# Performance work log

Measured on AMD Instinct MI355X. Metric: run time of the kernel, lower is better.

The kernel has to match this reference:

```python
import jax, jax.numpy as jnp
import numpy as np

DEPTH = 4
HEADS = 8
WINDOW = 256
RPW = 2                      # relay_tokens_per_window
SEQ_PER_RELAY = WINDOW // RPW  # 128 tokens per relay group
RELAY_START = 2              # depth_start_relay_attn (1-indexed layer number)
LN_EPS = 1e-5


def setup_inputs() -> dict:
    key = jax.random.key(0)
    ks = jax.random.split(key, 8)
    b, t, d, dff = 2, 2048, 512, 2048
    s = 0.02
    return {
        "x": jax.random.normal(ks[0], (b, t, d), dtype=jnp.float32),
        "relay_emb": jax.random.normal(ks[1], (1, d), dtype=jnp.float32) * s,
        "ln1_g": jnp.ones((DEPTH, d), jnp.float32),
        "ln1_b": jnp.zeros((DEPTH, d), jnp.float32),
        "loc_qkv_w": jax.random.normal(ks[2], (DEPTH, d, 3 * d), dtype=jnp.float32) * s,
        "loc_out_w": jax.random.normal(ks[3], (DEPTH, d, d), dtype=jnp.float32) * s,
        "loc_out_b": jnp.zeros((DEPTH, d), jnp.float32),
        "glob_qkv_w": jax.random.normal(ks[4], (DEPTH, d, 3 * d), dtype=jnp.float32) * s,
        "glob_out_w": jax.random.normal(ks[5], (DEPTH, d, d), dtype=jnp.float32) * s,
        "glob_out_b": jnp.zeros((DEPTH, d), jnp.float32),
        "ln2_g": jnp.ones((DEPTH, d), jnp.float32),
        "ln2_b": jnp.zeros((DEPTH, d), jnp.float32),
        "ff_w1": jax.random.normal(ks[6], (DEPTH, d, dff), dtype=jnp.float32) * s,
        "ff_b1": jnp.zeros((DEPTH, dff), jnp.float32),
        "ff_w2": jax.random.normal(ks[7], (DEPTH, dff, d), dtype=jnp.float32) * s,
        "ff_b2": jnp.zeros((DEPTH, d), jnp.float32),
    }


def _layernorm(x, g, b):
    m = jnp.mean(x, axis=-1, keepdims=True)
    v = jnp.mean(jnp.square(x - m), axis=-1, keepdims=True)
    return (x - m) * jax.lax.rsqrt(v + LN_EPS) * g + b


def _self_attention(x, qkv_w, out_w, out_b):
    # full (non-causal) multi-head attention, as in FullAttention
    b, t, d = x.shape
    h, dh = HEADS, d // HEADS
    q, k, v = jnp.split(x @ qkv_w, 3, axis=-1)
    mh = lambda u: u.reshape(b, t, h, dh).transpose(0, 2, 1, 3)  # b h t dh
    q, k, v = mh(q), mh(k), mh(v)
    dots = jnp.einsum('bhid,bhjd->bhij', q, k) * (dh ** -0.5)
    attn = jax.nn.softmax(dots, axis=-1)
    o = jnp.einsum('bhij,bhjd->bhid', attn, v)
    o = o.transpose(0, 2, 1, 3).reshape(b, t, d)
    return o @ out_w + out_b


def reference(x, relay_emb, ln1_g, ln1_b, loc_qkv_w, loc_out_w, loc_out_b,
              glob_qkv_w, glob_out_w, glob_out_b, ln2_g, ln2_b,
              ff_w1, ff_b1, ff_w2, ff_b2):
    b, t, d = x.shape
    # insert one relay token every SEQ_PER_RELAY tokens
    x = x.reshape(b, -1, SEQ_PER_RELAY, d)
    G = x.shape[1]
    rel = jnp.broadcast_to(relay_emb[None, None], (b, G, 1, d))
    x = jnp.concatenate([rel, x], axis=2).reshape(b, -1, d)  # (b, G*(129), d)

    for l in range(DEPTH):
        # attention block: PreNorm -> AttentionLayer, residual from sequence wrapper
        y = _layernorm(x, ln1_g[l], ln1_b[l])
        if (l + 1) >= RELAY_START:
            y = y.reshape(b, G, SEQ_PER_RELAY + 1, d)
            r = y[:, :, 0]                                       # (b, G, d) relay tokens
            r = _self_attention(r, glob_qkv_w[l], glob_out_w[l], glob_out_b[l]) + r
            y = jnp.concatenate([r[:, :, None], y[:, :, 1:]], axis=2).reshape(b, -1, d)
        x = x + _self_attention(y, loc_qkv_w[l], loc_out_w[l], loc_out_b[l])
        # feedforward block: PreNorm -> FFN with LeakyReLU(0.01)
        z = _layernorm(x, ln2_g[l], ln2_b[l])
        z = jax.nn.leaky_relu(z @ ff_w1[l] + ff_b1[l], negative_slope=0.01) @ ff_w2[l] + ff_b2[l]
        x = x + z

    # strip relay tokens
    x = x.reshape(b, G, SEQ_PER_RELAY + 1, d)
    return x[:, :, 1:].reshape(b, -1, d)
```

## Files before the change

### kernel.cpp

```cpp
#include <hip/hip_runtime.h>

typedef __attribute__((ext_vector_type(8))) __bf16 bf16x8;
typedef __attribute__((ext_vector_type(8))) unsigned short u16x8;
typedef __attribute__((ext_vector_type(4))) float f32x4;
typedef unsigned short u16;

#define TSEQ 2064
#define NTOK 4128
#define MPAD 4224

__device__ __forceinline__ float bf2f(u16 u) {
  unsigned x = ((unsigned)u) << 16;
  return __builtin_bit_cast(float, x);
}
__device__ __forceinline__ u16 f2bf(float f) {
  unsigned u = __builtin_bit_cast(unsigned, f);
  u += 0x7fffu + ((u >> 16) & 1u);
  return (u16)(u >> 16);
}

__device__ __forceinline__ void gll16(const u16* g, u16* l) {
  __builtin_amdgcn_global_load_lds((const __attribute__((address_space(1))) void*)g,
                                   (__attribute__((address_space(3))) void*)l, 16, 0, 0);
}
__device__ __forceinline__ int swz(int row, int col) {
  return row * 64 + (col ^ ((row & 7) << 3));
}

__global__ __launch_bounds__(256) void transpose_w(const float* __restrict__ src,
                                                   u16* __restrict__ dst,
                                                   int K, int N)
{
  __shared__ float tile[32][33];
  const int l = blockIdx.z;
  src += (size_t)l * K * N;
  dst += (size_t)l * K * N;
  const int n0 = blockIdx.x * 32, k0 = blockIdx.y * 32;
  const int c = threadIdx.x & 31, r = threadIdx.x >> 5;
#pragma unroll
  for (int rr = r; rr < 32; rr += 8)
    tile[rr][c] = src[(size_t)(k0 + rr) * N + n0 + c];
  __syncthreads();
#pragma unroll
  for (int rr = r; rr < 32; rr += 8)
    dst[(size_t)(n0 + rr) * K + k0 + c] = f2bf(tile[c][rr]);
}

__global__ void build_x(const float* __restrict__ xin, const float* __restrict__ relay,
                        float* __restrict__ xw)
{
  const int total = 2 * TSEQ * 512;
  for (int idx = blockIdx.x * 256 + threadIdx.x; idx < total; idx += gridDim.x * 256) {
    int col = idx & 511;
    int tok = (idx >> 9) % TSEQ;
    int b   = idx / (TSEQ * 512);
    int g = tok / 129, s = tok % 129;
    float v = (s == 0) ? relay[col]
                       : xin[((size_t)b * 2048 + g * 128 + (s - 1)) * 512 + col];
    xw[idx] = v;
  }
}

__global__ void extract_out(const float* __restrict__ xw, float* __restrict__ out)
{
  const int total = 2 * 2048 * 512;
  for (int idx = blockIdx.x * 256 + threadIdx.x; idx < total; idx += gridDim.x * 256) {
    int col = idx & 511;
    int tok = (idx >> 9) & 2047;
    int b   = idx / (2048 * 512);
    int g = tok >> 7, s = tok & 127;
    out[idx] = xw[((size_t)b * TSEQ + g * 129 + s + 1) * 512 + col];
  }
}

__global__ __launch_bounds__(256) void ln_kernel(const float* __restrict__ x,
                                                 const float* __restrict__ g,
                                                 const float* __restrict__ bta,
                                                 u16* __restrict__ y, int M)
{
  const int wid = threadIdx.x >> 6, lane = threadIdx.x & 63;
  const int row = blockIdx.x * 4 + wid;
  if (row >= M) return;
  const float* xr = x + (size_t)row * 512;
  float v[8];
  float s = 0.f;
#pragma unroll
  for (int j = 0; j < 8; ++j) { v[j] = xr[j * 64 + lane]; s += v[j]; }
#pragma unroll
  for (int m = 1; m <= 32; m <<= 1) s += __shfl_xor(s, m);
  float mean = s * (1.f / 512.f);
  float vs = 0.f;
#pragma unroll
  for (int j = 0; j < 8; ++j) { float d = v[j] - mean; vs += d * d; }
#pragma unroll
  for (int m = 1; m <= 32; m <<= 1) vs += __shfl_xor(vs, m);
  float rstd = rsqrtf(vs * (1.f / 512.f) + 1e-5f);
  u16* yr = y + (size_t)row * 512;
#pragma unroll
  for (int j = 0; j < 8; ++j) {
    int c = j * 64 + lane;
    yr[c] = f2bf((v[j] - mean) * rstd * g[c] + bta[c]);
  }
}

template<bool HAS_BIAS, bool ACT, bool RESID, bool OUT_BF16>
__global__ __launch_bounds__(256) void gemm2(
    const u16* __restrict__ A, const u16* __restrict__ Bt,
    const float* __restrict__ bias, const float* __restrict__ resid,
    void* __restrict__ outp, int M, int N, int K)
{
  __shared__ __attribute__((aligned(16))) u16 As[2][128 * 64];
  __shared__ __attribute__((aligned(16))) u16 Bs[2][128 * 64];
  const int tid = threadIdx.x, lane = tid & 63, wid = tid >> 6;
  const int row0 = blockIdx.x * 128, col0 = blockIdx.y * 128;
  const int wm = (wid >> 1) * 64, wn = (wid & 1) * 64;
  const int srow = tid >> 3, sseg = tid & 7;
  f32x4 acc[4][4];
#pragma unroll
  for (int m = 0; m < 4; ++m)
#pragma unroll
    for (int n = 0; n < 4; ++n) acc[m][n] = (f32x4)0.f;
  const u16* Ab = A + (size_t)row0 * K;
  const u16* Bb = Bt + (size_t)col0 * K;
#pragma unroll
  for (int i = 0; i < 4; ++i) {
    int row = srow + i * 32, ss = sseg ^ (row & 7);
    gll16(Ab + (size_t)row * K + ss * 8, &As[0][row * 64 + sseg * 8]);
    gll16(Bb + (size_t)row * K + ss * 8, &Bs[0][row * 64 + sseg * 8]);
  }
  const int fr = lane & 15, g = lane >> 4;
  int cur = 0;
  for (int k0 = 0; k0 < K; k0 += 64) {
    __syncthreads();
    if (k0 + 64 < K) {
      u16* ad = &As[cur ^ 1][0];
      u16* bd = &Bs[cur ^ 1][0];
#pragma unroll
      for (int i = 0; i < 4; ++i) {
        int row = srow + i * 32, ss = sseg ^ (row & 7);
        gll16(Ab + (size_t)row * K + k0 + 64 + ss * 8, ad + row * 64 + sseg * 8);
        gll16(Bb + (size_t)row * K + k0 + 64 + ss * 8, bd + row * 64 + sseg * 8);
      }
    }
    const u16* as_ = &As[cur][0];
    const u16* bs_ = &Bs[cur][0];
    bf16x8 a[2][4], bb[2][4];
#pragma unroll
    for (int kk = 0; kk < 2; ++kk) {
#pragma unroll
      for (int m = 0; m < 4; ++m) a[kk][m] = *(const bf16x8*)&as_[swz(wm + m * 16 + fr, kk * 32 + g * 8)];
#pragma unroll
      for (int n = 0; n < 4; ++n) bb[kk][n] = *(const bf16x8*)&bs_[swz(wn + n * 16 + fr, kk * 32 + g * 8)];
    }
    __builtin_amdgcn_s_setprio(1);
#pragma unroll
    for (int kk = 0; kk < 2; ++kk)
#pragma unroll
      for (int m = 0; m < 4; ++m)
#pragma unroll
        for (int n = 0; n < 4; ++n)
          acc[m][n] = __builtin_amdgcn_mfma_f32_16x16x32_bf16(a[kk][m], bb[kk][n], acc[m][n], 0, 0, 0);
    __builtin_amdgcn_s_setprio(0);
    cur ^= 1;
  }

  const int fg = lane >> 4;
#pragma unroll
  for (int m = 0; m < 4; ++m) {
#pragma unroll
    for (int n = 0; n < 4; ++n) {
#pragma unroll
      for (int j = 0; j < 4; ++j) {
        int grow = row0 + wm + m * 16 + fg * 4 + j;
        int gcol = col0 + wn + n * 16 + fr;
        if (grow < M) {
          float v = acc[m][n][j];
          if (HAS_BIAS) v += bias[gcol];
          if (ACT) v = (v > 0.f) ? v : 0.01f * v;
          if (RESID) v += resid[(size_t)grow * N + gcol];
          if (OUT_BF16) ((u16*)outp)[(size_t)grow * N + gcol] = f2bf(v);
          else ((float*)outp)[(size_t)grow * N + gcol] = v;
        }
      }
    }
  }
}

__global__ __launch_bounds__(256) void vtrans(const u16* __restrict__ big,
                                              u16* __restrict__ vg)
{
  __shared__ u16 t[64][72];
  const int tt = blockIdx.x;
  const int bh = blockIdx.y;
  const int b = bh >> 3, h = bh & 7;
  const int tid = threadIdx.x;
  const int srow = tid >> 3, sseg = tid & 7;
  const int t0 = tt * 64;
#pragma unroll
  for (int i = 0; i < 2; ++i) {
    int row = srow + i * 32;
    u16x8 v = *(const u16x8*)&big[((size_t)(b * TSEQ) + t0 + row) * 1536 + 1024 + h * 64 + sseg * 8];
    *(u16x8*)&t[row][sseg * 8] = v;
  }
  __syncthreads();
#pragma unroll
  for (int i = 0; i < 2; ++i) {
    int d = srow + i * 32;
    u16x8 v;
#pragma unroll
    for (int j = 0; j < 8; ++j) v[j] = t[sseg * 8 + j][d];
    *(u16x8*)&vg[((size_t)bh * 64 + d) * 2112 + t0 + sseg * 8] = v;
  }
}

__global__ __launch_bounds__(256) void flash_attn2(const u16* __restrict__ big,
                                                   const u16* __restrict__ vg,
                                                   u16* __restrict__ ob)
{
  __shared__ __attribute__((aligned(16))) u16 Qs[64 * 64];
  __shared__ __attribute__((aligned(16))) u16 Ks[2][64 * 64];
  __shared__ __attribute__((aligned(16))) u16 Vs[2][64 * 64];
  __shared__ __attribute__((aligned(16))) u16 Ps[4][16 * 64];
  const int tid = threadIdx.x, lane = tid & 63, wid = tid >> 6;
  const int qt = blockIdx.x, b = blockIdx.y >> 3, h = blockIdx.y & 7;
  const int q0 = qt * 64;
  const int srow = tid >> 3, sseg = tid & 7;

  const u16* qb = big + ((size_t)(b * TSEQ) + q0) * 1536 + h * 64;
  const u16* kb = big + ((size_t)(b * TSEQ)) * 1536 + h * 64 + 512;
  const u16* vb = vg + (size_t)blockIdx.y * 64 * 2112;
#pragma unroll
  for (int i = 0; i < 2; ++i) {
    int row = srow + i * 32, ss = sseg ^ (row & 7);
    gll16(qb + (size_t)row * 1536 + ss * 8, &Qs[row * 64 + sseg * 8]);
    gll16(kb + (size_t)row * 1536 + ss * 8, &Ks[0][row * 64 + sseg * 8]);
    gll16(vb + (size_t)row * 2112 + ss * 8, &Vs[0][row * 64 + sseg * 8]);
  }
  __syncthreads();
  const int fr = lane & 15, g = lane >> 4;
  bf16x8 aq0 = *(const bf16x8*)&Qs[swz(wid * 16 + fr, g * 8)];
  bf16x8 aq1 = *(const bf16x8*)&Qs[swz(wid * 16 + fr, 32 + g * 8)];

  f32x4 oacc[4];
#pragma unroll
  for (int nf = 0; nf < 4; ++nf) oacc[nf] = (f32x4)0.f;
  float mrow[4] = {-1e30f, -1e30f, -1e30f, -1e30f};
  float lsum[4] = {0.f, 0.f, 0.f, 0.f};
  int cur = 0;

  for (int kt = 0; kt < 33; ++kt) {
    if (kt + 1 < 33) {
      const u16* kb2 = kb + (size_t)(kt + 1) * 64 * 1536;
      const u16* vb2 = vb + (kt + 1) * 64;
      u16* kd = &Ks[cur ^ 1][0];
      u16* vd = &Vs[cur ^ 1][0];
#pragma unroll
      for (int i = 0; i < 2; ++i) {
        int row = srow + i * 32, ss = sseg ^ (row & 7);
        gll16(kb2 + (size_t)row * 1536 + ss * 8, kd + row * 64 + sseg * 8);
        gll16(vb2 + (size_t)row * 2112 + ss * 8, vd + row * 64 + sseg * 8);
      }
    }
    const u16* ks = &Ks[cur][0];
    const u16* vs = &Vs[cur][0];
    f32x4 s[4];
    __builtin_amdgcn_s_setprio(1);
#pragma unroll
    for (int n = 0; n < 4; ++n) {
      int row = n * 16 + fr;
      bf16x8 bk0 = *(const bf16x8*)&ks[swz(row, g * 8)];
      bf16x8 bk1 = *(const bf16x8*)&ks[swz(row, 32 + g * 8)];
      f32x4 t = (f32x4)0.f;
      t = __builtin_amdgcn_mfma_f32_16x16x32_bf16(aq0, bk0, t, 0, 0, 0);
      t = __builtin_amdgcn_mfma_f32_16x16x32_bf16(aq1, bk1, t, 0, 0, 0);
      s[n] = t;
    }
    __builtin_amdgcn_s_setprio(0);
#pragma unroll
    for (int n = 0; n < 4; ++n) {
      bool valid = (kt * 64 + n * 16 + fr) < TSEQ;
#pragma unroll
      for (int j = 0; j < 4; ++j) s[n][j] = valid ? s[n][j] * 0.125f : -1e30f;
    }
    float sc[4];
#pragma unroll
    for (int j = 0; j < 4; ++j) {
      float m0 = fmaxf(fmaxf(s[0][j], s[1][j]), fmaxf(s[2][j], s[3][j]));
#pragma unroll
      for (int d = 1; d <= 8; d <<= 1) m0 = fmaxf(m0, __shfl_xor(m0, d));
      float nm = fmaxf(mrow[j], m0);
      sc[j] = __expf(mrow[j] - nm);
      mrow[j] = nm;
      lsum[j] *= sc[j];
    }
#pragma unroll
    for (int nf = 0; nf < 4; ++nf)
#pragma unroll
      for (int j = 0; j < 4; ++j) oacc[nf][j] *= sc[j];

    float ps[4] = {0.f, 0.f, 0.f, 0.f};
#pragma unroll
    for (int n = 0; n < 4; ++n) {
#pragma unroll
      for (int j = 0; j < 4; ++j) {
        float p = __expf(s[n][j] - mrow[j]);
        ps[j] += p;
        Ps[wid][swz(g * 4 + j, n * 16 + fr)] = f2bf(p);
      }
    }
#pragma unroll
    for (int j = 0; j < 4; ++j) {
      float t = ps[j];
#pragma unroll
      for (int d = 1; d <= 8; d <<= 1) t += __shfl_xor(t, d);
      lsum[j] += t;
    }
    __builtin_amdgcn_s_setprio(1);
#pragma unroll
    for (int kc = 0; kc < 2; ++kc) {
      bf16x8 ap = *(const bf16x8*)&Ps[wid][swz(fr, kc * 32 + g * 8)];
#pragma unroll
      for (int nf = 0; nf < 4; ++nf) {
        bf16x8 bv = *(const bf16x8*)&vs[swz(nf * 16 + fr, kc * 32 + g * 8)];
        oacc[nf] = __builtin_amdgcn_mfma_f32_16x16x32_bf16(ap, bv, oacc[nf], 0, 0, 0);
      }
    }
    __builtin_amdgcn_s_setprio(0);
    __syncthreads();
    cur ^= 1;
  }

  float inv[4];
#pragma unroll
  for (int j = 0; j < 4; ++j) inv[j] = 1.f / lsum[j];
#pragma unroll
  for (int nf = 0; nf < 4; ++nf) {
#pragma unroll
    for (int j = 0; j < 4; ++j) {
      int row = q0 + wid * 16 + g * 4 + j;
      if (row < TSEQ)
        ob[((size_t)(b * TSEQ + row)) * 512 + h * 64 + nf * 16 + fr] = f2bf(oacc[nf][j] * inv[j]);
    }
  }
}

__global__ __launch_bounds__(256) void global_attn(const u16* __restrict__ rqkv,
                                                   u16* __restrict__ ro)
{
  const int b = blockIdx.x >> 3, h = blockIdx.x & 7;
  __shared__ float q[16][64], k[16][64], v[16][64], s[16][16], p[16][16];
  const int tid = threadIdx.x;
  for (int idx = tid; idx < 1024; idx += 256) {
    int rr = idx >> 6, c = idx & 63;
    size_t base = (size_t)(b * 16 + rr) * 1536 + h * 64 + c;
    q[rr][c] = bf2f(rqkv[base]);
    k[rr][c] = bf2f(rqkv[base + 512]);
    v[rr][c] = bf2f(rqkv[base + 1024]);
  }
  __syncthreads();
  {
    int i = tid >> 4, j = tid & 15;
    float acc = 0.f;
#pragma unroll
    for (int d = 0; d < 64; ++d) acc += q[i][d] * k[j][d];
    s[i][j] = acc * 0.125f;
  }
  __syncthreads();
  if (tid < 16) {
    float mx = -1e30f;
#pragma unroll
    for (int j = 0; j < 16; ++j) mx = fmaxf(mx, s[tid][j]);
    float sum = 0.f;
#pragma unroll
    for (int j = 0; j < 16; ++j) { float e = __expf(s[tid][j] - mx); p[tid][j] = e; sum += e; }
    float iv = 1.f / sum;
#pragma unroll
    for (int j = 0; j < 16; ++j) p[tid][j] *= iv;
  }
  __syncthreads();
  for (int idx = tid; idx < 1024; idx += 256) {
    int rr = idx >> 6, c = idx & 63;
    float acc = 0.f;
#pragma unroll
    for (int j = 0; j < 16; ++j) acc += p[rr][j] * v[j][c];
    ro[(size_t)(b * 16 + rr) * 512 + h * 64 + c] = f2bf(acc);
  }
}

__global__ void gather_relay(const u16* __restrict__ y, u16* __restrict__ rbuf)
{
  int idx = blockIdx.x * 256 + threadIdx.x;
  int col = idx & 511, rr = idx >> 9;
  int b = rr >> 4, g = rr & 15;
  rbuf[idx] = y[((size_t)b * TSEQ + g * 129) * 512 + col];
}

__global__ void relay_scatter(const float* __restrict__ rout, const u16* __restrict__ rbuf,
                              u16* __restrict__ y)
{
  int idx = blockIdx.x * 256 + threadIdx.x;
  int col = idx & 511, rr = idx >> 9;
  int b = rr >> 4, g = rr & 15;
  y[((size_t)b * TSEQ + g * 129) * 512 + col] = f2bf(rout[idx] + bf2f(rbuf[idx]));
}

extern "C" void kernel_launch(void* const* d_in, const int* in_sizes, int n_in,
                              void* d_out, int out_size, void* d_ws, size_t ws_size,
                              hipStream_t stream)
{
  const float* x_in     = (const float*)d_in[0];
  const float* rel_emb  = (const float*)d_in[1];
  const float* ln1_g    = (const float*)d_in[2];
  const float* ln1_b    = (const float*)d_in[3];
  const float* loc_qkv  = (const float*)d_in[4];
  const float* loc_ow   = (const float*)d_in[5];
  const float* loc_ob   = (const float*)d_in[6];
  const float* glob_qkv = (const float*)d_in[7];
  const float* glob_ow  = (const float*)d_in[8];
  const float* glob_ob  = (const float*)d_in[9];
  const float* ln2_g    = (const float*)d_in[10];
  const float* ln2_b    = (const float*)d_in[11];
  const float* ff_w1    = (const float*)d_in[12];
  const float* ff_b1    = (const float*)d_in[13];
  const float* ff_w2    = (const float*)d_in[14];
  const float* ff_b2    = (const float*)d_in[15];

  char* ws = (char*)d_ws;
  float* xbuf = (float*)(ws + 0);
  u16*   ybuf = (u16*)(ws + 8650752);
  u16*   obuf = (u16*)(ws + 12976128);
  u16*   big  = (u16*)(ws + 17301504);
  u16*   vg   = (u16*)(ws + 34603008);
  u16*   wLQ  = (u16*)(ws + 38928384);
  u16*   wGQ  = (u16*)(ws + 45219840);
  u16*   wLO  = (u16*)(ws + 51511296);
  u16*   wGO  = (u16*)(ws + 53608448);
  u16*   wF1  = (u16*)(ws + 55705600);
  u16*   wF2  = (u16*)(ws + 64094208);
  u16*   rbuf = (u16*)(ws + 72482816);
  u16*   rqkv = (u16*)(ws + 72613888);
  u16*   rov  = (u16*)(ws + 72712192);
  float* rout = (float*)(ws + 72843264);

  dim3 B(256);
  transpose_w<<<dim3(48, 16, 4), B, 0, stream>>>(loc_qkv, wLQ, 512, 1536);
  transpose_w<<<dim3(48, 16, 4), B, 0, stream>>>(glob_qkv, wGQ, 512, 1536);
  transpose_w<<<dim3(16, 16, 4), B, 0, stream>>>(loc_ow, wLO, 512, 512);
  transpose_w<<<dim3(16, 16, 4), B, 0, stream>>>(glob_ow, wGO, 512, 512);
  transpose_w<<<dim3(64, 16, 4), B, 0, stream>>>(ff_w1, wF1, 512, 2048);
  transpose_w<<<dim3(16, 64, 4), B, 0, stream>>>(ff_w2, wF2, 2048, 512);

  build_x<<<8256, B, 0, stream>>>(x_in, rel_emb, xbuf);

  for (int l = 0; l < 4; ++l) {
    ln_kernel<<<1032, B, 0, stream>>>(xbuf, ln1_g + l * 512, ln1_b + l * 512, ybuf, NTOK);
    if (l + 1 >= 2) {
      gather_relay<<<64, B, 0, stream>>>(ybuf, rbuf);
      gemm2<false, false, false, true><<<dim3(1, 12), B, 0, stream>>>(
          rbuf, wGQ + (size_t)l * 1536 * 512, nullptr, nullptr, rqkv, 32, 1536, 512);
      global_attn<<<16, B, 0, stream>>>(rqkv, rov);
      gemm2<true, false, false, false><<<dim3(1, 4), B, 0, stream>>>(
          rov, wGO + (size_t)l * 512 * 512, glob_ob + l * 512, nullptr, rout, 32, 512, 512);
      relay_scatter<<<64, B, 0, stream>>>(rout, rbuf, ybuf);
    }
    gemm2<false, false, false, true><<<dim3(33, 12), B, 0, stream>>>(
        ybuf, wLQ + (size_t)l * 1536 * 512, nullptr, nullptr, big, NTOK, 1536, 512);
    vtrans<<<dim3(33, 16), B, 0, stream>>>(big, vg);
    flash_attn2<<<dim3(33, 16), B, 0, stream>>>(big, vg, obuf);
    gemm2<true, false, true, false><<<dim3(33, 4), B, 0, stream>>>(
        obuf, wLO + (size_t)l * 512 * 512, loc_ob + l * 512, xbuf, xbuf, NTOK, 512, 512);
    ln_kernel<<<1032, B, 0, stream>>>(xbuf, ln2_g + l * 512, ln2_b + l * 512, ybuf, NTOK);
    gemm2<true, true, false, true><<<dim3(33, 16), B, 0, stream>>>(
        ybuf, wF1 + (size_t)l * 2048 * 512, ff_b1 + l * 2048, nullptr, big, NTOK, 2048, 512);
    gemm2<true, false, true, false><<<dim3(33, 4), B, 0, stream>>>(
        big, wF2 + (size_t)l * 512 * 2048, ff_b2 + l * 512, xbuf, xbuf, NTOK, 512, 2048);
  }
  extract_out<<<8192, B, 0, stream>>>(xbuf, (float*)d_out);
}
```

Baseline: 1.160 ms.

## Split flash attention over key range, fuse V transpose into QKV GEMM epilogue

The QKV projection GEMM now writes the V slice directly in transposed per-head layout, which removes the separate vtrans kernel. Flash attention is split into two halves along the key dimension (grid z=2), doubling the number of blocks. Each half writes unnormalized partial outputs plus per-row max and sum, and a new fa_combine kernel merges them. The softmax is reworked to compute S transposed (K as the A operand), so the row max and sum need fewer shuffles, and P is staged in the reused Q shared memory. The trade-offs are an extra combine pass, scattered 2-byte stores in the GEMM epilogue, and bf16 rounding of the unnormalized partial outputs.

```diff
diff --git a/kernel.cpp b/kernel.cpp
--- a/kernel.cpp
+++ b/kernel.cpp
@@ -2,6 +2,7 @@
 
 typedef __attribute__((ext_vector_type(8))) __bf16 bf16x8;
 typedef __attribute__((ext_vector_type(8))) unsigned short u16x8;
+typedef __attribute__((ext_vector_type(4))) unsigned short u16x4;
 typedef __attribute__((ext_vector_type(4))) float f32x4;
 typedef unsigned short u16;
 
@@ -103,11 +104,11 @@
   }
 }
 
-template<bool HAS_BIAS, bool ACT, bool RESID, bool OUT_BF16>
+template<bool HAS_BIAS, bool ACT, bool RESID, bool OUT_BF16, bool VOUT>
 __global__ __launch_bounds__(256) void gemm2(
     const u16* __restrict__ A, const u16* __restrict__ Bt,
     const float* __restrict__ bias, const float* __restrict__ resid,
-    void* __restrict__ outp, int M, int N, int K)
+    void* __restrict__ outp, u16* __restrict__ vgout, int M, int N, int K)
 {
   __shared__ __attribute__((aligned(16))) u16 As[2][128 * 64];
   __shared__ __attribute__((aligned(16))) u16 Bs[2][128 * 64];
@@ -164,92 +165,75 @@
     cur ^= 1;
   }
 
-  const int fg = lane >> 4;
 #pragma unroll
   for (int m = 0; m < 4; ++m) {
 #pragma unroll
     for (int n = 0; n < 4; ++n) {
 #pragma unroll
       for (int j = 0; j < 4; ++j) {
-        int grow = row0 + wm + m * 16 + fg * 4 + j;
+        int grow = row0 + wm + m * 16 + g * 4 + j;
         int gcol = col0 + wn + n * 16 + fr;
         if (grow < M) {
           float v = acc[m][n][j];
           if (HAS_BIAS) v += bias[gcol];
           if (ACT) v = (v > 0.f) ? v : 0.01f * v;
           if (RESID) v += resid[(size_t)grow * N + gcol];
-          if (OUT_BF16) ((u16*)outp)[(size_t)grow * N + gcol] = f2bf(v);
-          else ((float*)outp)[(size_t)grow * N + gcol] = v;
+          if (VOUT && gcol >= 1024) {
+            int hh = (gcol - 1024) >> 6, dd = gcol & 63;
+            int bb2 = grow >= TSEQ;
+            int tok = grow - bb2 * TSEQ;
+            vgout[((size_t)((bb2 * 8 + hh) * 64 + dd)) * 2112 + tok] = f2bf(v);
+          } else if (OUT_BF16) {
+            ((u16*)outp)[(size_t)grow * N + gcol] = f2bf(v);
+          } else {
+            ((float*)outp)[(size_t)grow * N + gcol] = v;
+          }
         }
       }
     }
   }
 }
 
-__global__ __launch_bounds__(256) void vtrans(const u16* __restrict__ big,
-                                              u16* __restrict__ vg)
-{
-  __shared__ u16 t[64][72];
-  const int tt = blockIdx.x;
-  const int bh = blockIdx.y;
-  const int b = bh >> 3, h = bh & 7;
-  const int tid = threadIdx.x;
-  const int srow = tid >> 3, sseg = tid & 7;
-  const int t0 = tt * 64;
-#pragma unroll
-  for (int i = 0; i < 2; ++i) {
-    int row = srow + i * 32;
-    u16x8 v = *(const u16x8*)&big[((size_t)(b * TSEQ) + t0 + row) * 1536 + 1024 + h * 64 + sseg * 8];
-    *(u16x8*)&t[row][sseg * 8] = v;
-  }
-  __syncthreads();
-#pragma unroll
-  for (int i = 0; i < 2; ++i) {
-    int d = srow + i * 32;
-    u16x8 v;
-#pragma unroll
-    for (int j = 0; j < 8; ++j) v[j] = t[sseg * 8 + j][d];
-    *(u16x8*)&vg[((size_t)bh * 64 + d) * 2112 + t0 + sseg * 8] = v;
-  }
-}
-
-__global__ __launch_bounds__(256) void flash_attn2(const u16* __restrict__ big,
+__global__ __launch_bounds__(256) void flash_attn3(const u16* __restrict__ big,
                                                    const u16* __restrict__ vg,
-                                                   u16* __restrict__ ob)
+                                                   u16* __restrict__ op0,
+                                                   u16* __restrict__ op1,
+                                                   float2* __restrict__ mlb)
 {
   __shared__ __attribute__((aligned(16))) u16 Qs[64 * 64];
   __shared__ __attribute__((aligned(16))) u16 Ks[2][64 * 64];
   __shared__ __attribute__((aligned(16))) u16 Vs[2][64 * 64];
-  __shared__ __attribute__((aligned(16))) u16 Ps[4][16 * 64];
   const int tid = threadIdx.x, lane = tid & 63, wid = tid >> 6;
-  const int qt = blockIdx.x, b = blockIdx.y >> 3, h = blockIdx.y & 7;
+  const int qt = blockIdx.x, bh = blockIdx.y, z = blockIdx.z;
+  const int b = bh >> 3, h = bh & 7;
   const int q0 = qt * 64;
   const int srow = tid >> 3, sseg = tid & 7;
+  const int ktbeg = z * 17, ktend = z ? 33 : 17;
 
   const u16* qb = big + ((size_t)(b * TSEQ) + q0) * 1536 + h * 64;
   const u16* kb = big + ((size_t)(b * TSEQ)) * 1536 + h * 64 + 512;
-  const u16* vb = vg + (size_t)blockIdx.y * 64 * 2112;
+  const u16* vb = vg + (size_t)bh * 64 * 2112;
 #pragma unroll
   for (int i = 0; i < 2; ++i) {
     int row = srow + i * 32, ss = sseg ^ (row & 7);
     gll16(qb + (size_t)row * 1536 + ss * 8, &Qs[row * 64 + sseg * 8]);
-    gll16(kb + (size_t)row * 1536 + ss * 8, &Ks[0][row * 64 + sseg * 8]);
-    gll16(vb + (size_t)row * 2112 + ss * 8, &Vs[0][row * 64 + sseg * 8]);
+    gll16(kb + (size_t)(ktbeg * 64 + row) * 1536 + ss * 8, &Ks[0][row * 64 + sseg * 8]);
+    gll16(vb + (size_t)row * 2112 + ktbeg * 64 + ss * 8, &Vs[0][row * 64 + sseg * 8]);
   }
   __syncthreads();
   const int fr = lane & 15, g = lane >> 4;
   bf16x8 aq0 = *(const bf16x8*)&Qs[swz(wid * 16 + fr, g * 8)];
   bf16x8 aq1 = *(const bf16x8*)&Qs[swz(wid * 16 + fr, 32 + g * 8)];
+  u16* Pw = &Qs[wid * 1024];
 
   f32x4 oacc[4];
 #pragma unroll
   for (int nf = 0; nf < 4; ++nf) oacc[nf] = (f32x4)0.f;
-  float mrow[4] = {-1e30f, -1e30f, -1e30f, -1e30f};
-  float lsum[4] = {0.f, 0.f, 0.f, 0.f};
+  float mrow = -1e30f, lsum = 0.f;
   int cur = 0;
 
-  for (int kt = 0; kt < 33; ++kt) {
-    if (kt + 1 < 33) {
+  for (int kt = ktbeg; kt < ktend; ++kt) {
+    if (kt + 1 < ktend) {
       const u16* kb2 = kb + (size_t)(kt + 1) * 64 * 1536;
       const u16* vb2 = vb + (kt + 1) * 64;
       u16* kd = &Ks[cur ^ 1][0];
@@ -268,57 +252,58 @@
 #pragma unroll
     for (int n = 0; n < 4; ++n) {
       int row = n * 16 + fr;
-      bf16x8 bk0 = *(const bf16x8*)&ks[swz(row, g * 8)];
-      bf16x8 bk1 = *(const bf16x8*)&ks[swz(row, 32 + g * 8)];
+      bf16x8 ak0 = *(const bf16x8*)&ks[swz(row, g * 8)];
+      bf16x8 ak1 = *(const bf16x8*)&ks[swz(row, 32 + g * 8)];
       f32x4 t = (f32x4)0.f;
-      t = __builtin_amdgcn_mfma_f32_16x16x32_bf16(aq0, bk0, t, 0, 0, 0);
-      t = __builtin_amdgcn_mfma_f32_16x16x32_bf16(aq1, bk1, t, 0, 0, 0);
+      t = __builtin_amdgcn_mfma_f32_16x16x32_bf16(ak0, aq0, t, 0, 0, 0);
+      t = __builtin_amdgcn_mfma_f32_16x16x32_bf16(ak1, aq1, t, 0, 0, 0);
       s[n] = t;
     }
     __builtin_amdgcn_s_setprio(0);
 #pragma unroll
     for (int n = 0; n < 4; ++n) {
-      bool valid = (kt * 64 + n * 16 + fr) < TSEQ;
-#pragma unroll
-      for (int j = 0; j < 4; ++j) s[n][j] = valid ? s[n][j] * 0.125f : -1e30f;
-    }
-    float sc[4];
-#pragma unroll
-    for (int j = 0; j < 4; ++j) {
-      float m0 = fmaxf(fmaxf(s[0][j], s[1][j]), fmaxf(s[2][j], s[3][j]));
-#pragma unroll
-      for (int d = 1; d <= 8; d <<= 1) m0 = fmaxf(m0, __shfl_xor(m0, d));
-      float nm = fmaxf(mrow[j], m0);
-      sc[j] = __expf(mrow[j] - nm);
-      mrow[j] = nm;
-      lsum[j] *= sc[j];
-    }
+      int kbase = kt * 64 + n * 16 + g * 4;
+#pragma unroll
+      for (int j = 0; j < 4; ++j)
+        s[n][j] = (kbase + j < TSEQ) ? s[n][j] * 0.125f : -1e30f;
+    }
+    float mloc = s[0][0];
+#pragma unroll
+    for (int n = 0; n < 4; ++n)
+#pragma unroll
+      for (int j = 0; j < 4; ++j) mloc = fmaxf(mloc, s[n][j]);
+    mloc = fmaxf(mloc, __shfl_xor(mloc, 16));
+    mloc = fmaxf(mloc, __shfl_xor(mloc, 32));
+    float nm = fmaxf(mrow, mloc);
+    float sc = __expf(mrow - nm);
+    mrow = nm;
+    lsum *= sc;
+    float psum = 0.f;
+#pragma unroll
+    for (int n = 0; n < 4; ++n) {
+      u16x4 pw;
+#pragma unroll
+      for (int j = 0; j < 4; ++j) {
+        float p = __expf(s[n][j] - nm);
+        psum += p;
+        pw[j] = f2bf(p);
+      }
+      *(u16x4*)&Pw[swz(fr, n * 16 + g * 4)] = pw;
+    }
+    psum += __shfl_xor(psum, 16);
+    psum += __shfl_xor(psum, 32);
+    lsum += psum;
+    float s4[4];
+#pragma unroll
+    for (int j = 0; j < 4; ++j) s4[j] = __shfl(sc, g * 4 + j);
 #pragma unroll
     for (int nf = 0; nf < 4; ++nf)
 #pragma unroll
-      for (int j = 0; j < 4; ++j) oacc[nf][j] *= sc[j];
-
-    float ps[4] = {0.f, 0.f, 0.f, 0.f};
-#pragma unroll
-    for (int n = 0; n < 4; ++n) {
-#pragma unroll
-      for (int j = 0; j < 4; ++j) {
-        float p = __expf(s[n][j] - mrow[j]);
-        ps[j] += p;
-        Ps[wid][swz(g * 4 + j, n * 16 + fr)] = f2bf(p);
-      }
-    }
-#pragma unroll
-    for (int j = 0; j < 4; ++j) {
-      float t = ps[j];
-#pragma unroll
-      for (int d = 1; d <= 8; d <<= 1) t += __shfl_xor(t, d);
-      lsum[j] += t;
-    }
+      for (int j = 0; j < 4; ++j) oacc[nf][j] *= s4[j];
     __builtin_amdgcn_s_setprio(1);
 #pragma unroll
     for (int kc = 0; kc < 2; ++kc) {
-      bf16x8 ap = *(const bf16x8*)&Ps[wid][swz(fr, kc * 32 + g * 8)];
+      bf16x8 ap = *(const bf16x8*)&Pw[swz(fr, kc * 32 + g * 8)];
 #pragma unroll
       for (int nf = 0; nf < 4; ++nf) {
         bf16x8 bv = *(const bf16x8*)&vs[swz(nf * 16 + fr, kc * 32 + g * 8)];
@@ -330,18 +315,46 @@
     cur ^= 1;
   }
 
-  float inv[4];
-#pragma unroll
-  for (int j = 0; j < 4; ++j) inv[j] = 1.f / lsum[j];
+  u16* op = z ? op1 : op0;
 #pragma unroll
   for (int nf = 0; nf < 4; ++nf) {
 #pragma unroll
     for (int j = 0; j < 4; ++j) {
       int row = q0 + wid * 16 + g * 4 + j;
       if (row < TSEQ)
-        ob[((size_t)(b * TSEQ + row)) * 512 + h * 64 + nf * 16 + fr] = f2bf(oacc[nf][j] * inv[j]);
-    }
-  }
+        op[((size_t)(b * TSEQ + row)) * 512 + h * 64 + nf * 16 + fr] = f2bf(oacc[nf][j]);
+    }
+  }
+  if (lane < 16) {
+    int row = q0 + wid * 16 + fr;
+    if (row < TSEQ)
+      mlb[(size_t)(z * 16 + bh) * 2112 + row] = float2{mrow, lsum};
+  }
+}
+
+__global__ __launch_bounds__(256) void fa_combine(const u16* __restrict__ op0,
+                                                  const u16* __restrict__ op1,
+                                                  const float2* __restrict__ mlb,
+                                                  u16* __restrict__ ob)
+{
+  int idx = blockIdx.x * 256 + threadIdx.x;
+  int tok = idx >> 7;
+  int c4 = (idx & 127) * 4;
+  int b = tok >= TSEQ;
+  int row = tok - b * TSEQ;
+  int h = c4 >> 6;
+  float2 ml0 = mlb[(size_t)(b * 8 + h) * 2112 + row];
+  float2 ml1 = mlb[(size_t)(16 + b * 8 + h) * 2112 + row];
+  float M = fmaxf(ml0.x, ml1.x);
+  float a0 = __expf(ml0.x - M), a1 = __expf(ml1.x - M);
+  float inv = 1.f / (ml0.y * a0 + ml1.y * a1);
+  u16x4 v0 = *(const u16x4*)&op0[(size_t)tok * 512 + c4];
+  u16x4 v1 = *(const u16x4*)&op1[(size_t)tok * 512 + c4];
+  u16x4 o;
+#pragma unroll
+  for (int j = 0; j < 4; ++j)
+    o[j] = f2bf((bf2f(v0[j]) * a0 + bf2f(v1[j]) * a1) * inv);
+  *(u16x4*)&ob[(size_t)tok * 512 + c4] = o;
 }
 
 __global__ __launch_bounds__(256) void global_attn(const u16* __restrict__ rqkv,
@@ -441,6 +454,7 @@
   u16*   rqkv = (u16*)(ws + 72613888);
   u16*   rov  = (u16*)(ws + 72712192);
   float* rout = (float*)(ws + 72843264);
+  float2* mlb = (float2*)(ws + 72908800);
 
   dim3 B(256);
   transpose_w<<<dim3(48, 16, 4), B, 0, stream>>>(loc_qkv, wLQ, 512, 1536);
@@ -456,24 +470,24 @@
     ln_kernel<<<1032, B, 0, stream>>>(xbuf, ln1_g + l * 512, ln1_b + l * 512, ybuf, NTOK);
     if (l + 1 >= 2) {
       gather_relay<<<64, B, 0, stream>>>(ybuf, rbuf);
-      gemm2<false, false, false, true><<<dim3(1, 12), B, 0, stream>>>(
-          rbuf, wGQ + (size_t)l * 1536 * 512, nullptr, nullptr, rqkv, 32, 1536, 512);
+      gemm2<false, false, false, true, false><<<dim3(1, 12), B, 0, stream>>>(
+          rbuf, wGQ + (size_t)l * 1536 * 512, nullptr, nullptr, rqkv, nullptr, 32, 1536, 512);
       global_attn<<<16, B, 0, stream>>>(rqkv, rov);
-      gemm2<true, false, false, false><<<dim3(1, 4), B, 0, stream>>>(
-          rov, wGO + (size_t)l * 512 * 512, glob_ob + l * 512, nullptr, rout, 32, 512, 512);
+      gemm2<true, false, false, false, false><<<dim3(1, 4), B, 0, stream>>>(
+          rov, wGO + (size_t)l * 512 * 512, glob_ob + l * 512, nullptr, rout, nullptr, 32, 512, 512);
       relay_scatter<<<64, B, 0, stream>>>(rout, rbuf, ybuf);
     }
-    gemm2<false, false, false, true><<<dim3(33, 12), B, 0, stream>>>(
-        ybuf, wLQ + (size_t)l * 1536 * 512, nullptr, nullptr, big, NTOK, 1536, 512);
-    vtrans<<<dim3(33, 16), B, 0, stream>>>(big, vg);
-    flash_attn2<<<dim3(33, 16), B, 0, stream>>>(big, vg, obuf);
-    gemm2<true, false, true, false><<<dim3(33, 4), B, 0, stream>>>(
-        obuf, wLO + (size_t)l * 512 * 512, loc_ob + l * 512, xbuf, xbuf, NTOK, 512, 512);
+    gemm2<false, false, false, true, true><<<dim3(33, 12), B, 0, stream>>>(
+        ybuf, wLQ + (size_t)l * 1536 * 512, nullptr, nullptr, big, vg, NTOK, 1536, 512);
+    flash_attn3<<<dim3(33, 16, 2), B, 0, stream>>>(big, vg, ybuf, obuf, mlb);
+    fa_combine<<<2064, B, 0, stream>>>(ybuf, obuf, mlb, obuf);
+    gemm2<true, false, true, false, false><<<dim3(33, 4), B, 0, stream>>>(
+        obuf, wLO + (size_t)l * 512 * 512, loc_ob + l * 512, xbuf, xbuf, nullptr, NTOK, 512, 512);
     ln_kernel<<<1032, B, 0, stream>>>(xbuf, ln2_g + l * 512, ln2_b + l * 512, ybuf, NTOK);
-    gemm2<true, true, false, true><<<dim3(33, 16), B, 0, stream>>>(
-        ybuf, wF1 + (size_t)l * 2048 * 512, ff_b1 + l * 2048, nullptr, big, NTOK, 2048, 512);
-    gemm2<true, false, true, false><<<dim3(33, 4), B, 0, stream>>>(
-        big, wF2 + (size_t)l * 512 * 2048, ff_b2 + l * 512, xbuf, xbuf, NTOK, 512, 2048);
+    gemm2<true, true, false, true, false><<<dim3(33, 16), B, 0, stream>>>(
+        ybuf, wF1 + (size_t)l * 2048 * 512, ff_b1 + l * 2048, nullptr, big, nullptr, NTOK, 2048, 512);
+    gemm2<true, false, true, false, false><<<dim3(33, 4), B, 0, stream>>>(
+        big, wF2 + (size_t)l * 512 * 2048, ff_b2 + l * 512, xbuf, xbuf, nullptr, NTOK, 512, 2048);
   }
   extract_out<<<8192, B, 0, stream>>>(xbuf, (float*)d_out);
 }
```

Result: faster. 1.071 ms (-7.7%).
